# Kernel tuning notes

Measured on AMD Instinct MI355X. Metric: run time of the kernel, lower is better.

The kernel has to match this reference:

```python
import jax, jax.numpy as jnp
import numpy as np

N_NODES = 40000
N_EDGES = 640000
D_FEAT = 128


def setup_inputs() -> dict:
    key = jax.random.key(0)
    k1, k2, k3, k4 = jax.random.split(key, 4)
    rows = jax.random.randint(k1, (N_EDGES,), 0, N_NODES, dtype=jnp.int32)
    cols = jax.random.randint(k2, (N_EDGES,), 0, N_NODES, dtype=jnp.int32)
    vals = jax.random.uniform(k3, (N_EDGES,), dtype=jnp.float32)
    annotations = jax.random.normal(k4, (N_NODES, D_FEAT), dtype=jnp.float32)
    return {"rows": rows, "cols": cols, "vals": vals, "annotations": annotations}


def reference(rows, cols, vals, annotations):
    # out = adjacent @ annotations, with adjacent given in COO form:
    # adjacent[rows[e], cols[e]] = vals[e].
    # SpMM as gather -> scale -> segment_sum over destination rows.
    gathered = annotations[cols] * vals[:, None]          # [E, d]
    out = jax.ops.segment_sum(gathered, rows, num_segments=N_NODES)  # [N, d]
    return out
```

## Files before the change

### kernel.cpp

```cpp
#include <hip/hip_runtime.h>


constexpr int N_NODES = 40000;
constexpr int N_EDGES = 640000;
constexpr int D_FEAT  = 128;
constexpr int CAP     = 32;
constexpr int OVF_CAP = 16384;
constexpr int CSTR    = 16;

constexpr int NXCD      = 8;
constexpr int PART_ROWS = N_NODES / NXCD;
constexpr int EPT       = 10;
constexpr int CHUNK     = 256 * EPT;
constexpr int NCHUNK    = N_EDGES / CHUNK;
constexpr int SCAT_BLOCKS = NCHUNK * NXCD;
constexpr int CONV_BLOCKS = (N_NODES * D_FEAT / 8) / 256;

constexpr size_t WS_CURSOR = 0;
constexpr size_t WS_OVFCNT = 2560000;
constexpr size_t WS_OVF    = 2560256;
constexpr size_t WS_ANNB   = 2822400;
constexpr size_t WS_PAIRS  = 13062400;
constexpr size_t WS_ZERO   = 2560256;
constexpr size_t WS_NEEDED = 23302400;

typedef int      v2i __attribute__((ext_vector_type(2)));
typedef float    v2f __attribute__((ext_vector_type(2)));
typedef float    v4f __attribute__((ext_vector_type(4)));
typedef unsigned v4u __attribute__((ext_vector_type(4)));

__device__ __forceinline__ unsigned f2b_rne(float f) {
    unsigned b = __float_as_uint(f);
    return (b + 0x7fffu + ((b >> 16) & 1u)) >> 16;
}

__global__ __launch_bounds__(256) void build_kernel(
    const int*   __restrict__ rows,
    const int*   __restrict__ cols,
    const float* __restrict__ vals,
    const float* __restrict__ ann,
    unsigned*    __restrict__ annb,
    int* __restrict__ cursor, v2i* __restrict__ pairs,
    int* __restrict__ ovfcnt, int4* __restrict__ ovf)
{
    if (blockIdx.x < SCAT_BLOCKS) {
        int p     = blockIdx.x & 7;
        int chunk = blockIdx.x >> 3;
        int e0    = chunk * CHUNK + threadIdx.x;

        int   r[EPT], c[EPT];
        float v[EPT];
        #pragma unroll
        for (int i = 0; i < EPT; i++) {
            int e = e0 + i * 256;
            r[i] = __builtin_nontemporal_load(rows + e);
            c[i] = __builtin_nontemporal_load(cols + e);
            v[i] = __builtin_nontemporal_load(vals + e);
        }
        #pragma unroll
        for (int i = 0; i < EPT; i++) {
            if (r[i] / PART_ROWS != p) continue;
            int slot = atomicAdd(&cursor[r[i] * CSTR], 1);
            if (slot < CAP) {
                v2i q;
                q.x = c[i];
                q.y = __float_as_int(v[i]);
                pairs[r[i] * CAP + slot] = q;
            } else {
                int o = atomicAdd(ovfcnt, 1);
                if (o < OVF_CAP)
                    ovf[o] = make_int4(r[i], c[i], __float_as_int(v[i]), 0);
            }
        }
    } else {
        int t = (blockIdx.x - SCAT_BLOCKS) * 256 + threadIdx.x;
        v4f f0 = __builtin_nontemporal_load(reinterpret_cast<const v4f*>(ann) + 2 * t);
        v4f f1 = __builtin_nontemporal_load(reinterpret_cast<const v4f*>(ann) + 2 * t + 1);
        v4u o;
        o.x = f2b_rne(f0.x) | (f2b_rne(f0.y) << 16);
        o.y = f2b_rne(f0.z) | (f2b_rne(f0.w) << 16);
        o.z = f2b_rne(f1.x) | (f2b_rne(f1.y) << 16);
        o.w = f2b_rne(f1.z) | (f2b_rne(f1.w) << 16);
        reinterpret_cast<v4u*>(annb)[t] = o;
    }
}

__global__ __launch_bounds__(256) void pull_kernel(
    const unsigned* __restrict__ annb,
    const int*      __restrict__ cursor,
    const v2i*      __restrict__ pairs,
    const int*      __restrict__ ovfcnt,
    const int4*     __restrict__ ovf,
    float*          __restrict__ out)
{
    int B = blockIdx.x;
    int L = (B & 7) * 1250 + (B >> 3);
    int r    = L * 4 + (threadIdx.x >> 6);
    int lane = threadIdx.x & 63;

    int cntr = cursor[r * CSTR];
    int cnt  = cntr > CAP ? CAP : cntr;

    int2 pr = make_int2(0, 0);
    if (lane < cnt) {
        v2i p = pairs[r * CAP + lane];
        pr.x = p.x;
        pr.y = p.y;
    }

    float2 acc = make_float2(0.f, 0.f);
    int nb = (cnt + 7) & ~7;
    for (int j = 0; j < nb; j += 8) {
        #pragma unroll
        for (int k = 0; k < 8; k++) {
            int      c = __shfl(pr.x, j + k, 64);
            float    v = __int_as_float(__shfl(pr.y, j + k, 64));
            unsigned p = annb[c * (D_FEAT / 2) + lane];
            acc.x += v * __uint_as_float(p << 16);
            acc.y += v * __uint_as_float(p & 0xffff0000u);
        }
    }

    if (cntr > CAP) {
        int n = *ovfcnt;
        n = n > OVF_CAP ? OVF_CAP : n;
        for (int i = 0; i < n; i++) {
            int4 e = ovf[i];
            if (e.x == r) {
                unsigned p = annb[e.y * (D_FEAT / 2) + lane];
                float    v = __int_as_float(e.z);
                acc.x += v * __uint_as_float(p << 16);
                acc.y += v * __uint_as_float(p & 0xffff0000u);
            }
        }
    }

    v2f o;
    o.x = acc.x;
    o.y = acc.y;
    __builtin_nontemporal_store(
        o, reinterpret_cast<v2f*>(out) + ((size_t)r * (D_FEAT / 2) + lane));
}

__global__ __launch_bounds__(256) void spmm_scatter_kernel(
    const int*   __restrict__ rows,
    const int*   __restrict__ cols,
    const float* __restrict__ vals,
    const float* __restrict__ ann,
    float*       __restrict__ out)
{
    int t = blockIdx.x * blockDim.x + threadIdx.x;
    int e = t >> 5;
    if (e >= N_EDGES) return;
    int lane = t & 31;
    int   r = rows[e];
    int   c = cols[e];
    float v = vals[e];
    float4 a = reinterpret_cast<const float4*>(ann)[(size_t)c * (D_FEAT / 4) + lane];
    float* o = out + (size_t)r * D_FEAT + lane * 4;
    unsafeAtomicAdd(o + 0, v * a.x);
    unsafeAtomicAdd(o + 1, v * a.y);
    unsafeAtomicAdd(o + 2, v * a.z);
    unsafeAtomicAdd(o + 3, v * a.w);
}

extern "C" void kernel_launch(void* const* d_in, const int* in_sizes, int n_in,
                              void* d_out, int out_size, void* d_ws, size_t ws_size,
                              hipStream_t stream) {
    const int*   rows = (const int*)  d_in[0];
    const int*   cols = (const int*)  d_in[1];
    const float* vals = (const float*)d_in[2];
    const float* ann  = (const float*)d_in[3];
    float*       out  = (float*)      d_out;

    if (ws_size < WS_NEEDED) {
        hipMemsetAsync(out, 0, (size_t)out_size * sizeof(float), stream);
        const long long total_threads = (long long)N_EDGES * 32;
        spmm_scatter_kernel<<<dim3((unsigned)((total_threads + 255) / 256)),
                              dim3(256), 0, stream>>>(rows, cols, vals, ann, out);
        return;
    }

    char*     ws     = (char*)d_ws;
    int*      cursor = (int*)     (ws + WS_CURSOR);
    int*      ovfcnt = (int*)     (ws + WS_OVFCNT);
    int4*     ovf    = (int4*)    (ws + WS_OVF);
    unsigned* annb   = (unsigned*)(ws + WS_ANNB);
    v2i*      pairs  = (v2i*)     (ws + WS_PAIRS);

    hipMemsetAsync(cursor, 0, WS_ZERO, stream);

    build_kernel<<<dim3(SCAT_BLOCKS + CONV_BLOCKS), dim3(256), 0, stream>>>(
        rows, cols, vals, ann, annb, cursor, pairs, ovfcnt, ovf);

    const long long pull_threads = (long long)N_NODES * 64;
    pull_kernel<<<dim3((unsigned)((pull_threads + 255) / 256)), dim3(256), 0, stream>>>(
        annb, cursor, pairs, ovfcnt, ovf, out);
}
```

Before: 135.7 us.

## Add partition pass bucketing edges by row partition before per-row scatter

Adds a kernel that bins edges into 8 row-partition buckets using shared-memory counters and one global atomic per bucket per block. The build kernel then reads only its own partition's bucket instead of every block re-reading all edges and discarding 7/8 of them. This cuts redundant edge reads in the build step. In exchange it adds an extra kernel launch and writes and reads a 16-byte-per-edge intermediate list, plus a second overflow path.

```diff
diff --git a/kernel.cpp b/kernel.cpp
--- a/kernel.cpp
+++ b/kernel.cpp
@@ -10,21 +10,29 @@
 
 constexpr int NXCD      = 8;
 constexpr int PART_ROWS = N_NODES / NXCD;
-constexpr int EPT       = 10;
-constexpr int CHUNK     = 256 * EPT;
-constexpr int NCHUNK    = N_EDGES / CHUNK;
-constexpr int SCAT_BLOCKS = NCHUNK * NXCD;
+constexpr int BUCK_CAP  = 96000;
+constexpr int OVF2_CAP  = 4096;
+
+constexpr int A_EPT    = 2;
+constexpr int A_BLOCKS = N_EDGES / (256 * A_EPT);
+constexpr int B_GROUP  = 320;
+constexpr int B_BLOCKS = B_GROUP * NXCD;
 constexpr int CONV_BLOCKS = (N_NODES * D_FEAT / 8) / 256;
 
-constexpr size_t WS_CURSOR = 0;
-constexpr size_t WS_OVFCNT = 2560000;
-constexpr size_t WS_OVF    = 2560256;
-constexpr size_t WS_ANNB   = 2822400;
-constexpr size_t WS_PAIRS  = 13062400;
-constexpr size_t WS_ZERO   = 2560256;
-constexpr size_t WS_NEEDED = 23302400;
+constexpr size_t WS_CURSOR  = 0;
+constexpr size_t WS_OVFCNT  = 2560000;
+constexpr size_t WS_GCNT    = 2560064;
+constexpr size_t WS_OVF2CNT = 2560576;
+constexpr size_t WS_OVF     = 2560640;
+constexpr size_t WS_OVF2    = 2822784;
+constexpr size_t WS_ANNB    = 2888320;
+constexpr size_t WS_ELIST   = 13128320;
+constexpr size_t WS_PAIRS   = 25416320;
+constexpr size_t WS_NEEDED  = 35656320;
+constexpr size_t WS_ZERO    = 2560580;
 
 typedef int      v2i __attribute__((ext_vector_type(2)));
+typedef int      v4i __attribute__((ext_vector_type(4)));
 typedef float    v2f __attribute__((ext_vector_type(2)));
 typedef float    v4f __attribute__((ext_vector_type(4)));
 typedef unsigned v4u __attribute__((ext_vector_type(4)));
@@ -34,46 +42,105 @@
     return (b + 0x7fffu + ((b >> 16) & 1u)) >> 16;
 }
 
-__global__ __launch_bounds__(256) void build_kernel(
+__global__ __launch_bounds__(256) void partition_kernel(
     const int*   __restrict__ rows,
     const int*   __restrict__ cols,
     const float* __restrict__ vals,
+    int* __restrict__ gcnt,
+    v4i* __restrict__ elist,
+    int* __restrict__ ovf2cnt, v4i* __restrict__ ovf2)
+{
+    __shared__ int s_cnt[NXCD];
+    __shared__ int s_base[NXCD];
+    int tid = threadIdx.x;
+    if (tid < NXCD) s_cnt[tid] = 0;
+    __syncthreads();
+
+    int e0 = blockIdx.x * (256 * A_EPT) + tid;
+    int   r[A_EPT], c[A_EPT], rk[A_EPT], b[A_EPT];
+    float v[A_EPT];
+    #pragma unroll
+    for (int i = 0; i < A_EPT; i++) {
+        int e = e0 + i * 256;
+        r[i] = __builtin_nontemporal_load(rows + e);
+        c[i] = __builtin_nontemporal_load(cols + e);
+        v[i] = __builtin_nontemporal_load(vals + e);
+        b[i] = r[i] / PART_ROWS;
+        rk[i] = atomicAdd(&s_cnt[b[i]], 1);
+    }
+    __syncthreads();
+    if (tid < NXCD) s_base[tid] = atomicAdd(&gcnt[tid * CSTR], s_cnt[tid]);
+    __syncthreads();
+
+    #pragma unroll
+    for (int i = 0; i < A_EPT; i++) {
+        int pos = s_base[b[i]] + rk[i];
+        v4i e4;
+        e4.x = r[i];
+        e4.y = c[i];
+        e4.z = __float_as_int(v[i]);
+        e4.w = 0;
+        if (pos < BUCK_CAP) {
+            elist[(size_t)b[i] * BUCK_CAP + pos] = e4;
+        } else {
+            int o = atomicAdd(ovf2cnt, 1);
+            if (o < OVF2_CAP) ovf2[o] = e4;
+        }
+    }
+}
+
+__device__ __forceinline__ void scatter_to_row(
+    int r, int c, float v, int* cursor, v2i* pairs,
+    int* ovfcnt, v4i* ovf)
+{
+    int slot = atomicAdd(&cursor[r * CSTR], 1);
+    if (slot < CAP) {
+        v2i q;
+        q.x = c;
+        q.y = __float_as_int(v);
+        pairs[r * CAP + slot] = q;
+    } else {
+        int o = atomicAdd(ovfcnt, 1);
+        if (o < OVF_CAP) {
+            v4i e4;
+            e4.x = r; e4.y = c; e4.z = __float_as_int(v); e4.w = 0;
+            ovf[o] = e4;
+        }
+    }
+}
+
+__global__ __launch_bounds__(256) void build_kernel(
     const float* __restrict__ ann,
     unsigned*    __restrict__ annb,
+    const int*   __restrict__ gcnt,
+    const v4i*   __restrict__ elist,
     int* __restrict__ cursor, v2i* __restrict__ pairs,
-    int* __restrict__ ovfcnt, int4* __restrict__ ovf)
-{
-    if (blockIdx.x < SCAT_BLOCKS) {
-        int p     = blockIdx.x & 7;
-        int chunk = blockIdx.x >> 3;
-        int e0    = chunk * CHUNK + threadIdx.x;
-
-        int   r[EPT], c[EPT];
-        float v[EPT];
-        #pragma unroll
-        for (int i = 0; i < EPT; i++) {
-            int e = e0 + i * 256;
-            r[i] = __builtin_nontemporal_load(rows + e);
-            c[i] = __builtin_nontemporal_load(cols + e);
-            v[i] = __builtin_nontemporal_load(vals + e);
-        }
-        #pragma unroll
-        for (int i = 0; i < EPT; i++) {
-            if (r[i] / PART_ROWS != p) continue;
-            int slot = atomicAdd(&cursor[r[i] * CSTR], 1);
-            if (slot < CAP) {
-                v2i q;
-                q.x = c[i];
-                q.y = __float_as_int(v[i]);
-                pairs[r[i] * CAP + slot] = q;
-            } else {
-                int o = atomicAdd(ovfcnt, 1);
-                if (o < OVF_CAP)
-                    ovf[o] = make_int4(r[i], c[i], __float_as_int(v[i]), 0);
+    int* __restrict__ ovfcnt, v4i* __restrict__ ovf,
+    const int* __restrict__ ovf2cnt, const v4i* __restrict__ ovf2)
+{
+    if (blockIdx.x < B_BLOCKS) {
+        int p = blockIdx.x & 7;
+        int k = blockIdx.x >> 3;
+        int tid = threadIdx.x;
+
+        int cnt = gcnt[p * CSTR];
+        cnt = cnt > BUCK_CAP ? BUCK_CAP : cnt;
+
+        for (int i = k * 256 + tid; i < cnt; i += B_GROUP * 256) {
+            v4i e = __builtin_nontemporal_load(elist + ((size_t)p * BUCK_CAP + i));
+            scatter_to_row(e.x, e.y, __int_as_float(e.z), cursor, pairs, ovfcnt, ovf);
+        }
+
+        if (p == 0 && k == 0) {
+            int n = *ovf2cnt;
+            n = n > OVF2_CAP ? OVF2_CAP : n;
+            for (int i = tid; i < n; i += 256) {
+                v4i e = ovf2[i];
+                scatter_to_row(e.x, e.y, __int_as_float(e.z), cursor, pairs, ovfcnt, ovf);
             }
         }
     } else {
-        int t = (blockIdx.x - SCAT_BLOCKS) * 256 + threadIdx.x;
+        int t = (blockIdx.x - B_BLOCKS) * 256 + threadIdx.x;
         v4f f0 = __builtin_nontemporal_load(reinterpret_cast<const v4f*>(ann) + 2 * t);
         v4f f1 = __builtin_nontemporal_load(reinterpret_cast<const v4f*>(ann) + 2 * t + 1);
         v4u o;
@@ -90,7 +157,7 @@
     const int*      __restrict__ cursor,
     const v2i*      __restrict__ pairs,
     const int*      __restrict__ ovfcnt,
-    const int4*     __restrict__ ovf,
+    const v4i*      __restrict__ ovf,
     float*          __restrict__ out)
 {
     int B = blockIdx.x;
@@ -125,7 +192,7 @@
         int n = *ovfcnt;
         n = n > OVF_CAP ? OVF_CAP : n;
         for (int i = 0; i < n; i++) {
-            int4 e = ovf[i];
+            v4i e = ovf[i];
             if (e.x == r) {
                 unsigned p = annb[e.y * (D_FEAT / 2) + lane];
                 float    v = __int_as_float(e.z);
@@ -181,17 +248,24 @@
         return;
     }
 
-    char*     ws     = (char*)d_ws;
-    int*      cursor = (int*)     (ws + WS_CURSOR);
-    int*      ovfcnt = (int*)     (ws + WS_OVFCNT);
-    int4*     ovf    = (int4*)    (ws + WS_OVF);
-    unsigned* annb   = (unsigned*)(ws + WS_ANNB);
-    v2i*      pairs  = (v2i*)     (ws + WS_PAIRS);
+    char*     ws      = (char*)d_ws;
+    int*      cursor  = (int*)     (ws + WS_CURSOR);
+    int*      ovfcnt  = (int*)     (ws + WS_OVFCNT);
+    int*      gcnt    = (int*)     (ws + WS_GCNT);
+    int*      ovf2cnt = (int*)     (ws + WS_OVF2CNT);
+    v4i*      ovf     = (v4i*)     (ws + WS_OVF);
+    v4i*      ovf2    = (v4i*)     (ws + WS_OVF2);
+    unsigned* annb    = (unsigned*)(ws + WS_ANNB);
+    v4i*      elist   = (v4i*)     (ws + WS_ELIST);
+    v2i*      pairs   = (v2i*)     (ws + WS_PAIRS);
 
     hipMemsetAsync(cursor, 0, WS_ZERO, stream);
 
-    build_kernel<<<dim3(SCAT_BLOCKS + CONV_BLOCKS), dim3(256), 0, stream>>>(
-        rows, cols, vals, ann, annb, cursor, pairs, ovfcnt, ovf);
+    partition_kernel<<<dim3(A_BLOCKS), dim3(256), 0, stream>>>(
+        rows, cols, vals, gcnt, elist, ovf2cnt, ovf2);
+
+    build_kernel<<<dim3(B_BLOCKS + CONV_BLOCKS), dim3(256), 0, stream>>>(
+        ann, annb, gcnt, elist, cursor, pairs, ovfcnt, ovf, ovf2cnt, ovf2);
 
     const long long pull_threads = (long long)N_NODES * 64;
     pull_kernel<<<dim3((unsigned)((pull_threads + 255) / 256)), dim3(256), 0, stream>>>(
```

Result: slower. 162.1 us (+19.5%).
